# Kernel optimization log

Measured on AMD Instinct MI355X. Metric: run time of the kernel, lower is better.

## Reference

```python
import jax, jax.numpy as jnp
import numpy as np

T, B, V = 2048, 256, 90   # max_length, batch, pitch classes
P = V - 1                 # 89 pattern channels
IGNORE = 999
EPS = 1e-28


def setup_inputs() -> dict:
    key = jax.random.key(0)
    k1, k2, k3, k4, k5 = jax.random.split(key, 5)
    return {
        "first_scores": jax.random.normal(k1, (T, B, V), dtype=jnp.float32),
        "pattern_scores": jax.random.uniform(k2, (T, B, P), dtype=jnp.float32),
        "first_targs": jax.random.randint(k3, (T, B), 0, V),
        "pattern_targs": jax.random.uniform(k4, (T, B, P), dtype=jnp.float32),
        "lengths": jax.random.randint(k5, (B,), 0, T),
    }


def reference(first_scores, pattern_scores, first_targs, pattern_targs, lengths):
    # CrossEntropyLoss(reduction='none', ignore_index=999) on [T*B, 90] -> [T, B]
    logp = jax.nn.log_softmax(first_scores, axis=-1)
    valid = (first_targs != IGNORE)
    targs_c = jnp.clip(first_targs, 0, V - 1)
    first_losses = -jnp.take_along_axis(logp, targs_c[..., None], axis=-1)[..., 0]
    first_losses = first_losses * valid.astype(first_losses.dtype)

    # Vectorized mask: mask[j, i, k] = 1 iff j < lengths[i] and k < 89 - first_targs[j, i]
    k = jnp.arange(P)                                             # [P]
    len_mask = jnp.arange(T)[:, None] < lengths[None, :]          # [T, B]
    mask = (k[None, None, :] < (P - first_targs)[:, :, None]) & len_mask[:, :, None]
    mask = mask.astype(pattern_scores.dtype)

    # Masked BCE over pattern channels
    pattern_losses = -(pattern_targs * jnp.log(pattern_scores + EPS)
                       + (1.0 - pattern_targs) * jnp.log(1.0 - pattern_scores + EPS))
    pattern_losses = (pattern_losses * mask).sum(axis=2)          # [T, B]

    losses = first_losses + pattern_losses
    return losses.sum() / B
```

## Files before the change

### kernel.cpp

```cpp
#include <hip/hip_runtime.h>

constexpr int T = 2048;
constexpr int B = 256;
constexpr int V = 90;
constexpr int P = 89;
constexpr int IGNORE = 999;
constexpr float EPS = 1e-28f;

__global__ __launch_bounds__(256) void trans_inv_loss_kernel(
    const float* __restrict__ first_scores,
    const float* __restrict__ pattern_scores,
    const int*   __restrict__ first_targs,
    const float* __restrict__ pattern_targs,
    const int*   __restrict__ lengths,
    float*       __restrict__ out)
{
    const int row = blockIdx.x * blockDim.x + threadIdx.x;

    float loss = 0.0f;

    if (row < T * B) {
        const int t = row >> 8;
        const int b = row & (B - 1);

        const int targ = first_targs[row];
        const int len  = lengths[b];

        const float* fs = first_scores + (size_t)row * V;
        float st = fs[targ];
        float s = 0.0f;
        #pragma unroll 9
        for (int j = 0; j < V / 2; ++j) {
            const float2 x = *(const float2*)(fs + 2 * j);
            s += __expf(x.x) + __expf(x.y);
        }
        if (targ != IGNORE)
            loss = __logf(s) - st;

        if (t < len) {
            const int kmax = P - targ;
            const float* ps = pattern_scores + (size_t)row * P;
            const float* pt = pattern_targs  + (size_t)row * P;
            #pragma unroll 4
            for (int k = 0; k < kmax; ++k) {
                float p = ps[k];
                float y = pt[k];
                float l1 = __logf(p + EPS);
                float l2 = __logf(1.0f - p + EPS);
                loss -= y * (l1 - l2) + l2;
            }
        }
    }

    #pragma unroll
    for (int off = 32; off > 0; off >>= 1)
        loss += __shfl_xor(loss, off, 64);

    __shared__ float warp_sums[4];
    const int lane = threadIdx.x & 63;
    const int wid  = threadIdx.x >> 6;
    if (lane == 0) warp_sums[wid] = loss;
    __syncthreads();

    if (threadIdx.x == 0) {
        float s = warp_sums[0] + warp_sums[1] + warp_sums[2] + warp_sums[3];
        atomicAdd(out, s * (1.0f / (float)B));
    }
}

extern "C" void kernel_launch(void* const* d_in, const int* in_sizes, int n_in,
                              void* d_out, int out_size, void* d_ws, size_t ws_size,
                              hipStream_t stream) {
    const float* first_scores   = (const float*)d_in[0];
    const float* pattern_scores = (const float*)d_in[1];
    const int*   first_targs    = (const int*)  d_in[2];
    const float* pattern_targs  = (const float*)d_in[3];
    const int*   lengths        = (const int*)  d_in[4];
    float* out = (float*)d_out;

    hipMemsetAsync(out, 0, sizeof(float) * (size_t)out_size, stream);

    dim3 block(256);
    dim3 grid((T * B + 255) / 256);
    trans_inv_loss_kernel<<<grid, block, 0, stream>>>(
        first_scores, pattern_scores, first_targs, pattern_targs, lengths, out);
}
```

Before: 501.6 us.

## Process one row per wavefront with coalesced lane loads and software prefetch

The kernel moves from one thread per row to one wavefront per row, iterating over 64 rows. Lanes read contiguous elements of each row, so global loads are coalesced instead of strided per thread. The next row's data is loaded before the current row is computed, a software-pipelined prefetch meant to hide memory latency. In exchange, each row now needs cross-lane shuffle reductions, lanes sit idle past 45 or 89 elements, and the grid is 64x smaller, which may reduce occupancy.

```diff
diff --git a/kernel.cpp b/kernel.cpp
--- a/kernel.cpp
+++ b/kernel.cpp
@@ -7,6 +7,8 @@
 constexpr int IGNORE = 999;
 constexpr float EPS = 1e-28f;
 
+constexpr int RPW = 64;
+
 __global__ __launch_bounds__(256) void trans_inv_loss_kernel(
     const float* __restrict__ first_scores,
     const float* __restrict__ pattern_scores,
@@ -15,57 +17,123 @@
     const int*   __restrict__ lengths,
     float*       __restrict__ out)
 {
-    const int row = blockIdx.x * blockDim.x + threadIdx.x;
+    const int lane  = threadIdx.x & 63;
+    const int gwave = (blockIdx.x * blockDim.x + threadIdx.x) >> 6;
+    const int r0    = gwave * RPW;
 
-    float loss = 0.0f;
+    const int tv   = first_targs[r0 + lane];
+    const int lenv = lengths[(r0 & (B - 1)) + lane];
+    const int t    = r0 >> 8;
 
-    if (row < T * B) {
-        const int t = row >> 8;
-        const int b = row & (B - 1);
+    float acc = 0.0f;
 
-        const int targ = first_targs[row];
-        const int len  = lengths[b];
+    int    targ = __shfl(tv, 0, 64);
+    int    len  = __shfl(lenv, 0, 64);
+    float2 x    = make_float2(0.0f, 0.0f);
+    {
+        const float* fs = first_scores + (size_t)r0 * V;
+        if (lane < 45) x = *(const float2*)(fs + 2 * lane);
+    }
+    float p0 = 0.f, y0 = 0.f, p1 = 0.f, y1 = 0.f;
+    {
+        const int kmax = P - targ;
+        if (t < len) {
+            const float* ps = pattern_scores + (size_t)r0 * P;
+            const float* pt = pattern_targs  + (size_t)r0 * P;
+            if (lane < kmax)      { p0 = ps[lane];      y0 = pt[lane];      }
+            if (lane + 64 < kmax) { p1 = ps[lane + 64]; y1 = pt[lane + 64]; }
+        }
+    }
 
-        const float* fs = first_scores + (size_t)row * V;
-        float st = fs[targ];
-        float s = 0.0f;
-        #pragma unroll 9
-        for (int j = 0; j < V / 2; ++j) {
-            const float2 x = *(const float2*)(fs + 2 * j);
-            s += __expf(x.x) + __expf(x.y);
+    #pragma unroll 2
+    for (int i = 0; i < RPW - 1; ++i) {
+        const int    targn = __shfl(tv, i + 1, 64);
+        const int    lenn  = __shfl(lenv, i + 1, 64);
+        const size_t rn    = (size_t)(r0 + i + 1);
+        float2 xn = make_float2(0.0f, 0.0f);
+        {
+            const float* fsn = first_scores + rn * V;
+            if (lane < 45) xn = *(const float2*)(fsn + 2 * lane);
         }
-        if (targ != IGNORE)
-            loss = __logf(s) - st;
+        float p0n = 0.f, y0n = 0.f, p1n = 0.f, y1n = 0.f;
+        {
+            const int kmaxn = P - targn;
+            if (t < lenn) {
+                const float* psn = pattern_scores + rn * P;
+                const float* ptn = pattern_targs  + rn * P;
+                if (lane < kmaxn)      { p0n = psn[lane];      y0n = ptn[lane];      }
+                if (lane + 64 < kmaxn) { p1n = psn[lane + 64]; y1n = ptn[lane + 64]; }
+            }
+        }
 
+        float e = (lane < 45) ? (__expf(x.x) + __expf(x.y)) : 0.0f;
+        #pragma unroll
+        for (int off = 32; off > 0; off >>= 1)
+            e += __shfl_xor(e, off, 64);
+        if (targ != IGNORE) {
+            const int   sl  = targ >> 1;
+            const float stx = __shfl(x.x, sl, 64);
+            const float sty = __shfl(x.y, sl, 64);
+            if (lane == 0)
+                acc += __logf(e) - ((targ & 1) ? sty : stx);
+        }
+        {
+            const int kmax = P - targ;
+            if (t < len) {
+                if (lane < kmax) {
+                    const float l1 = __logf(p0 + EPS);
+                    const float l2 = __logf(1.0f - p0 + EPS);
+                    acc -= y0 * (l1 - l2) + l2;
+                }
+                if (lane + 64 < kmax) {
+                    const float l1 = __logf(p1 + EPS);
+                    const float l2 = __logf(1.0f - p1 + EPS);
+                    acc -= y1 * (l1 - l2) + l2;
+                }
+            }
+        }
+
+        targ = targn; len = lenn; x = xn;
+        p0 = p0n; y0 = y0n; p1 = p1n; y1 = y1n;
+    }
+
+    {
+        float e = (lane < 45) ? (__expf(x.x) + __expf(x.y)) : 0.0f;
+        #pragma unroll
+        for (int off = 32; off > 0; off >>= 1)
+            e += __shfl_xor(e, off, 64);
+        if (targ != IGNORE) {
+            const int   sl  = targ >> 1;
+            const float stx = __shfl(x.x, sl, 64);
+            const float sty = __shfl(x.y, sl, 64);
+            if (lane == 0)
+                acc += __logf(e) - ((targ & 1) ? sty : stx);
+        }
+        const int kmax = P - targ;
         if (t < len) {
-            const int kmax = P - targ;
-            const float* ps = pattern_scores + (size_t)row * P;
-            const float* pt = pattern_targs  + (size_t)row * P;
-            #pragma unroll 4
-            for (int k = 0; k < kmax; ++k) {
-                float p = ps[k];
-                float y = pt[k];
-                float l1 = __logf(p + EPS);
-                float l2 = __logf(1.0f - p + EPS);
-                loss -= y * (l1 - l2) + l2;
+            if (lane < kmax) {
+                const float l1 = __logf(p0 + EPS);
+                const float l2 = __logf(1.0f - p0 + EPS);
+                acc -= y0 * (l1 - l2) + l2;
+            }
+            if (lane + 64 < kmax) {
+                const float l1 = __logf(p1 + EPS);
+                const float l2 = __logf(1.0f - p1 + EPS);
+                acc -= y1 * (l1 - l2) + l2;
             }
         }
     }
 
     #pragma unroll
     for (int off = 32; off > 0; off >>= 1)
-        loss += __shfl_xor(loss, off, 64);
+        acc += __shfl_xor(acc, off, 64);
 
-    __shared__ float warp_sums[4];
-    const int lane = threadIdx.x & 63;
-    const int wid  = threadIdx.x >> 6;
-    if (lane == 0) warp_sums[wid] = loss;
+    __shared__ float wsum[4];
+    const int wid = threadIdx.x >> 6;
+    if (lane == 0) wsum[wid] = acc;
     __syncthreads();
-
-    if (threadIdx.x == 0) {
-        float s = warp_sums[0] + warp_sums[1] + warp_sums[2] + warp_sums[3];
-        atomicAdd(out, s * (1.0f / (float)B));
-    }
+    if (threadIdx.x == 0)
+        atomicAdd(out, (wsum[0] + wsum[1] + wsum[2] + wsum[3]) * (1.0f / (float)B));
 }
 
 extern "C" void kernel_launch(void* const* d_in, const int* in_sizes, int n_in,
@@ -81,7 +149,7 @@
     hipMemsetAsync(out, 0, sizeof(float) * (size_t)out_size, stream);
 
     dim3 block(256);
-    dim3 grid((T * B + 255) / 256);
+    dim3 grid((T * B) / (256 / 64 * RPW));
     trans_inv_loss_kernel<<<grid, block, 0, stream>>>(
         first_scores, pattern_scores, first_targs, pattern_targs, lengths, out);
 }
```

After: 463.1 us. 7.7% less time.

## Stage row data through LDS with coalesced wave-wide loads and DPP reduction

Applied to the files above, without the earlier changes.

Replaces the per-thread strided row reads with a wave-cooperative scheme: each wave of 64 rows loads 16-column chunks in a coalesced pattern, transposes them through padded LDS buffers, and each lane then reads its own row. The pattern loop exits early via ballot once no lane still needs columns, and the cross-lane reduction uses DPP row operations instead of shuffles. The goal is to cut uncoalesced global traffic on a bandwidth-bound kernel. The cost is extra LDS traffic, masked wasted work, and tail clamping logic at the buffer end.

```diff
diff --git a/kernel.cpp b/kernel.cpp
--- a/kernel.cpp
+++ b/kernel.cpp
@@ -7,6 +7,25 @@
 constexpr int IGNORE = 999;
 constexpr float EPS = 1e-28f;
 
+constexpr size_t SZ_FS = (size_t)T * B * V;
+constexpr size_t SZ_P  = (size_t)T * B * P;
+constexpr int PAD = 18;
+
+template <int CTRL>
+__device__ __forceinline__ float dpp_add(float v) {
+    int t = __builtin_amdgcn_update_dpp(0, __float_as_int(v), CTRL, 0xf, 0xf, true);
+    return v + __int_as_float(t);
+}
+__device__ __forceinline__ float wave_sum_uniform(float v) {
+    v = dpp_add<0x111>(v);
+    v = dpp_add<0x112>(v);
+    v = dpp_add<0x114>(v);
+    v = dpp_add<0x118>(v);
+    v = dpp_add<0x142>(v);
+    v = dpp_add<0x143>(v);
+    return __int_as_float(__builtin_amdgcn_readlane(__float_as_int(v), 63));
+}
+
 __global__ __launch_bounds__(256) void trans_inv_loss_kernel(
     const float* __restrict__ first_scores,
     const float* __restrict__ pattern_scores,
@@ -15,57 +34,100 @@
     const int*   __restrict__ lengths,
     float*       __restrict__ out)
 {
-    const int row = blockIdx.x * blockDim.x + threadIdx.x;
+    const int lane  = threadIdx.x & 63;
+    const int wid   = threadIdx.x >> 6;
+    const int gwave = blockIdx.x * 4 + wid;
+    const int r0    = gwave * 64;
+    const int row   = r0 + lane;
+    const int t     = r0 >> 8;
 
-    float loss = 0.0f;
+    __shared__ float lds[4][2][64 * PAD];
+    float* bufA = lds[wid][0];
+    float* bufB = lds[wid][1];
 
-    if (row < T * B) {
-        const int t = row >> 8;
-        const int b = row & (B - 1);
+    const int   targ  = first_targs[row];
+    const int   len   = lengths[row & (B - 1)];
+    const int   ct    = ((unsigned)targ < (unsigned)V) ? targ : 0;
+    const float xt    = first_scores[(size_t)row * V + ct];
+    const int   km    = P - targ;
+    const int   ekmax = (t < len) ? (km > 0 ? km : 0) : 0;
 
-        const int targ = first_targs[row];
-        const int len  = lengths[b];
+    const int srow = lane >> 3;
+    const int scol = (lane & 7) * 2;
 
-        const float* fs = first_scores + (size_t)row * V;
-        float st = fs[targ];
-        float s = 0.0f;
-        #pragma unroll 9
-        for (int j = 0; j < V / 2; ++j) {
-            const float2 x = *(const float2*)(fs + 2 * j);
-            s += __expf(x.x) + __expf(x.y);
+    const float* fs_t = first_scores + (size_t)r0 * V;
+    float s = 0.0f;
+    #pragma unroll
+    for (int ck = 0; ck < 6; ++ck) {
+        const int c0 = ck * 16;
+        float2 tmp[8];
+        #pragma unroll
+        for (int k = 0; k < 8; ++k) {
+            size_t e = (size_t)(k * 8 + srow) * V + (c0 + scol);
+            if (ck == 5) {
+                size_t eg = (size_t)r0 * V + e;
+                if (eg > SZ_FS - 2) e -= (eg - (SZ_FS - 2));
+            }
+            tmp[k] = *(const float2*)(fs_t + e);
         }
-        if (targ != IGNORE)
-            loss = __logf(s) - st;
+        #pragma unroll
+        for (int k = 0; k < 8; ++k)
+            *(float2*)&bufA[(k * 8 + srow) * PAD + scol] = tmp[k];
+        __asm__ volatile("s_waitcnt lgkmcnt(0)" ::: "memory");
+        #pragma unroll
+        for (int j = 0; j < 8; ++j) {
+            if (ck == 5 && j >= 5) break;
+            float2 v = *(const float2*)&bufA[lane * PAD + 2 * j];
+            s += __expf(v.x) + __expf(v.y);
+        }
+    }
+    float acc = (targ != IGNORE) ? (__logf(s) - xt) : 0.0f;
 
-        if (t < len) {
-            const int kmax = P - targ;
-            const float* ps = pattern_scores + (size_t)row * P;
-            const float* pt = pattern_targs  + (size_t)row * P;
-            #pragma unroll 4
-            for (int k = 0; k < kmax; ++k) {
-                float p = ps[k];
-                float y = pt[k];
-                float l1 = __logf(p + EPS);
-                float l2 = __logf(1.0f - p + EPS);
-                loss -= y * (l1 - l2) + l2;
+    const float* ps_t = pattern_scores + (size_t)r0 * P;
+    const float* pt_t = pattern_targs  + (size_t)r0 * P;
+    #pragma unroll
+    for (int ck = 0; ck < 6; ++ck) {
+        const int c0 = ck * 16;
+        if (__ballot(ekmax > c0) == 0) break;
+        float a0[8], a1[8], b0[8], b1[8];
+        #pragma unroll
+        for (int k = 0; k < 8; ++k) {
+            size_t e = (size_t)(k * 8 + srow) * P + (c0 + scol);
+            if (ck == 5) {
+                size_t eg = (size_t)r0 * P + e;
+                if (eg > SZ_P - 2) e -= (eg - (SZ_P - 2));
             }
+            a0[k] = ps_t[e]; a1[k] = ps_t[e + 1];
+            b0[k] = pt_t[e]; b1[k] = pt_t[e + 1];
+        }
+        #pragma unroll
+        for (int k = 0; k < 8; ++k) {
+            *(float2*)&bufA[(k * 8 + srow) * PAD + scol] = make_float2(a0[k], a1[k]);
+            *(float2*)&bufB[(k * 8 + srow) * PAD + scol] = make_float2(b0[k], b1[k]);
+        }
+        __asm__ volatile("s_waitcnt lgkmcnt(0)" ::: "memory");
+        #pragma unroll
+        for (int j = 0; j < 8; ++j) {
+            float2 p = *(const float2*)&bufA[lane * PAD + 2 * j];
+            float2 y = *(const float2*)&bufB[lane * PAD + 2 * j];
+            const int c = c0 + 2 * j;
+            float l1 = __logf(p.x + EPS);
+            float l2 = __logf(1.0f - p.x + EPS);
+            float v0 = y.x * (l1 - l2) + l2;
+            float l3 = __logf(p.y + EPS);
+            float l4 = __logf(1.0f - p.y + EPS);
+            float v1 = y.y * (l3 - l4) + l4;
+            if (c < ekmax)     acc -= v0;
+            if (c + 1 < ekmax) acc -= v1;
         }
     }
 
-    #pragma unroll
-    for (int off = 32; off > 0; off >>= 1)
-        loss += __shfl_xor(loss, off, 64);
-
-    __shared__ float warp_sums[4];
-    const int lane = threadIdx.x & 63;
-    const int wid  = threadIdx.x >> 6;
-    if (lane == 0) warp_sums[wid] = loss;
+    const float wtot = wave_sum_uniform(acc);
+    __shared__ float wsum[4];
+    if (lane == 0) wsum[wid] = wtot;
     __syncthreads();
-
-    if (threadIdx.x == 0) {
-        float s = warp_sums[0] + warp_sums[1] + warp_sums[2] + warp_sums[3];
-        atomicAdd(out, s * (1.0f / (float)B));
-    }
+    if (threadIdx.x == 0)
+        atomicAdd(out, (wsum[0] + wsum[1] + wsum[2] + wsum[3]) * (1.0f / (float)B));
 }
 
 extern "C" void kernel_launch(void* const* d_in, const int* in_sizes, int n_in,
@@ -78,10 +140,10 @@
     const int*   lengths        = (const int*)  d_in[4];
     float* out = (float*)d_out;
 
-    hipMemsetAsync(out, 0, sizeof(float) * (size_t)out_size, stream);
+    (void)hipMemsetAsync(out, 0, sizeof(float) * (size_t)out_size, stream);
 
     dim3 block(256);
-    dim3 grid((T * B + 255) / 256);
+    dim3 grid((T * B) / (4 * 64));
     trans_inv_loss_kernel<<<grid, block, 0, stream>>>(
         first_scores, pattern_scores, first_targs, pattern_targs, lengths, out);
 }
```

Measured after the change: 554.5 us. 1.11x slower.
